# Kernel tuning notes

Measured on AMD Instinct MI355X. Metric: run time of the kernel, lower is better.

## Reference

```python
import jax, jax.numpy as jnp
import numpy as np


def _gcn_conv(x, src, dst, norm, W, b, n_nodes):
    # x: [N, Fin] -> [N, Fout]. PyG GCNConv: linear (no bias), normalized
    # scatter-add aggregation over edges (self-loops already in src/dst), + bias.
    h = x @ W                                  # [N, Fout]
    msg = h[src] * norm[:, None]               # [E+N, Fout]
    out = jax.ops.segment_sum(msg, dst, num_segments=n_nodes)
    return out + b


def _prep_edges(edge_index, n_nodes):
    # Add self-loops and compute symmetric normalization deg^-1/2 * deg^-1/2.
    loops = jnp.arange(n_nodes, dtype=edge_index.dtype)
    src = jnp.concatenate([edge_index[0], loops])
    dst = jnp.concatenate([edge_index[1], loops])
    deg = jax.ops.segment_sum(jnp.ones_like(dst, dtype=jnp.float32), dst,
                              num_segments=n_nodes)
    dinv = jnp.where(deg > 0, jax.lax.rsqrt(jnp.maximum(deg, 1.0)), 0.0)
    norm = dinv[src] * dinv[dst]
    return src, dst, norm


def setup_inputs() -> dict:
    key = jax.random.key(0)
    k1, k2, k3, k4 = jax.random.split(key, 4)
    N, Fin, Fout = 50000, 128, 64
    H = 2 * Fout
    E = 640000
    x = jax.random.normal(k1, (N, Fin), dtype=jnp.float32)
    edge_index = jax.random.randint(k2, (2, E), 0, N, dtype=jnp.int64)
    W1 = jax.random.normal(k3, (Fin, H), dtype=jnp.float32) * (1.0 / np.sqrt(Fin))
    b1 = jnp.zeros((H,), dtype=jnp.float32)
    W2 = jax.random.normal(k4, (H, Fout), dtype=jnp.float32) * (1.0 / np.sqrt(H))
    b2 = jnp.zeros((Fout,), dtype=jnp.float32)
    return {"x": x, "edge_index": edge_index, "W1": W1, "b1": b1, "W2": W2, "b2": b2}


def reference(x, edge_index, W1, b1, W2, b2):
    n_nodes = x.shape[0]
    src, dst, norm = _prep_edges(edge_index, n_nodes)
    h = _gcn_conv(x, src, dst, norm, W1, b1, n_nodes)
    h = jax.nn.relu(h)
    return _gcn_conv(h, src, dst, norm, W2, b2, n_nodes)
```

## Files before the change

### kernel.cpp

```cpp
#include <hip/hip_runtime.h>

#define CEILDIV(a,b) (((a)+(b)-1)/(b))

constexpr int BKCAP  = 1536;
constexpr int MAXBK  = 1024;
constexpr int CHUNKA = 4096;


__device__ __forceinline__ unsigned short f2bf(float f) {
  union { float f; unsigned u; } v; v.f = f;
  unsigned u = v.u + (0x7fffu + ((v.u >> 16) & 1u));
  return (unsigned short)(u >> 16);
}
__device__ __forceinline__ unsigned pack2(float lo, float hi) {
  return (unsigned)f2bf(lo) | ((unsigned)f2bf(hi) << 16);
}
__device__ __forceinline__ void add2(float* a, unsigned w) {
  union { unsigned u; float f; } lo, hi;
  lo.u = w << 16; hi.u = w & 0xffff0000u;
  a[0] += lo.f; a[1] += hi.f;
}
__device__ __forceinline__ void add8(float* a, uint4 w) {
  add2(a + 0, w.x); add2(a + 2, w.y); add2(a + 4, w.z); add2(a + 6, w.w);
}
__device__ __forceinline__ void fma2(float* a, unsigned w, float s) {
  union { unsigned u; float f; } lo, hi;
  lo.u = w << 16; hi.u = w & 0xffff0000u;
  a[0] = fmaf(lo.f, s, a[0]); a[1] = fmaf(hi.f, s, a[1]);
}
__device__ __forceinline__ void fma8(float* a, uint4 w, float s) {
  fma2(a + 0, w.x, s); fma2(a + 2, w.y, s); fma2(a + 4, w.z, s); fma2(a + 6, w.w, s);
}


__global__ __launch_bounds__(256) void k_init(const int* __restrict__ raw,
                                              int* __restrict__ ctrl, int E) {
  const int tid = threadIdx.x;
  for (int i = 1 + tid; i < 8 + MAXBK; i += 256) ctrl[i] = 0;
  __shared__ int ok;
  if (tid == 0) ok = 1;
  __syncthreads();
  int n = (E < 1024) ? E : 1024;
  for (int i = tid; i < n; i += 256)
    if (raw[2 * i + 1] != 0) ok = 0;
  __syncthreads();
  if (tid == 0) ctrl[0] = ok;
}

template <int K, int NO, bool XBF16, bool SCALE>
__device__ __forceinline__ void gemm_body(const void* __restrict__ Xv,
                                          const float* __restrict__ W,
                                          const int* __restrict__ cnt,
                                          unsigned short* __restrict__ Y,
                                          int N, int bid) {
  constexpr int ROWS = 128, KC = 16, TC = NO / 16;
  constexpr int XST = ROWS + 4;
  constexpr int WST = NO + 4;
  __shared__ float xs[KC * XST];
  __shared__ float ws[KC * WST];
  const int tid = threadIdx.x;
  const int tx = tid & 15, ty = tid >> 4;
  const int r0 = ty * 8;
  const int row0 = bid * ROWS;

  float acc[8][TC];
#pragma unroll
  for (int i = 0; i < 8; ++i)
#pragma unroll
    for (int j = 0; j < TC; ++j) acc[i][j] = 0.0f;

  for (int kk = 0; kk < K; kk += KC) {
#pragma unroll
    for (int it = 0; it < (ROWS * KC / 4) / 256; ++it) {
      int idx = it * 256 + tid;
      int r = idx >> 2, kq = idx & 3;
      int row = row0 + r; if (row >= N) row = N - 1;
      float f0, f1, f2, f3;
      if constexpr (XBF16) {
        const unsigned short* Xb = (const unsigned short*)Xv;
        uint2 v = *(const uint2*)&Xb[(size_t)row * K + kk + kq * 4];
        union { unsigned u; float f; } t0, t1, t2, t3;
        t0.u = v.x << 16; t1.u = v.x & 0xffff0000u;
        t2.u = v.y << 16; t3.u = v.y & 0xffff0000u;
        f0 = t0.f; f1 = t1.f; f2 = t2.f; f3 = t3.f;
      } else {
        const float* Xf = (const float*)Xv;
        float4 v = *(const float4*)&Xf[(size_t)row * K + kk + kq * 4];
        f0 = v.x; f1 = v.y; f2 = v.z; f3 = v.w;
      }
      xs[(kq * 4 + 0) * XST + r] = f0;
      xs[(kq * 4 + 1) * XST + r] = f1;
      xs[(kq * 4 + 2) * XST + r] = f2;
      xs[(kq * 4 + 3) * XST + r] = f3;
    }
#pragma unroll
    for (int it = 0; it < (KC * NO / 4) / 256; ++it) {
      int idx = it * 256 + tid;
      int c4 = idx & (NO / 4 - 1), kw = idx / (NO / 4);
      float4 v = *(const float4*)&W[(size_t)(kk + kw) * NO + c4 * 4];
      *(float4*)&ws[kw * WST + c4 * 4] = v;
    }
    __syncthreads();
#pragma unroll
    for (int k = 0; k < KC; ++k) {
      const float4 xa = *(const float4*)&xs[k * XST + r0];
      const float4 xb = *(const float4*)&xs[k * XST + r0 + 4];
      float4 wv[TC / 4];
      wv[0] = *(const float4*)&ws[k * WST + tx * 4];
      if constexpr (TC == 8)
        wv[1] = *(const float4*)&ws[k * WST + 64 + tx * 4];
      const float xr[8] = {xa.x, xa.y, xa.z, xa.w, xb.x, xb.y, xb.z, xb.w};
#pragma unroll
      for (int i = 0; i < 8; ++i)
#pragma unroll
        for (int j4 = 0; j4 < TC / 4; ++j4) {
          acc[i][j4 * 4 + 0] += xr[i] * wv[j4].x;
          acc[i][j4 * 4 + 1] += xr[i] * wv[j4].y;
          acc[i][j4 * 4 + 2] += xr[i] * wv[j4].z;
          acc[i][j4 * 4 + 3] += xr[i] * wv[j4].w;
        }
    }
    __syncthreads();
  }
#pragma unroll
  for (int i = 0; i < 8; ++i) {
    int r = row0 + r0 + i;
    if (r < N) {
      const float dv = SCALE ? rsqrtf((float)(cnt[r] + 1)) : 1.0f;
      uint2 pa = make_uint2(pack2(acc[i][0] * dv, acc[i][1] * dv),
                            pack2(acc[i][2] * dv, acc[i][3] * dv));
      *(uint2*)&Y[(size_t)r * NO + tx * 4] = pa;
      if constexpr (TC == 8) {
        uint2 pb = make_uint2(pack2(acc[i][4] * dv, acc[i][5] * dv),
                              pack2(acc[i][6] * dv, acc[i][7] * dv));
        *(uint2*)&Y[(size_t)r * NO + 64 + tx * 4] = pb;
      }
    }
  }
}

__global__ __launch_bounds__(256, 4) void k_work1(
    const float* __restrict__ X, const float* __restrict__ W1,
    unsigned short* __restrict__ hb1, int N, int FA,
    const int* __restrict__ raw, int* __restrict__ ctrl,
    unsigned* __restrict__ ebuf, int E, int nbk) {
  const int i = blockIdx.x;
  if (i >= FA) {
    gemm_body<128, 128, false, false>(X, W1, nullptr, hb1, N, i - FA);
    return;
  }
  __shared__ int lcnt[MAXBK], lbase[MAXBK], lrank[MAXBK];
  const int tid = threadIdx.x;
  for (int b = tid; b < nbk; b += 256) { lcnt[b] = 0; lrank[b] = 0; }
  __syncthreads();
  const bool is64 = (ctrl[0] != 0);
  const int e0 = i * CHUNKA;
  const int e1 = min(E, e0 + CHUNKA);
  for (int e = e0 + tid; e < e1; e += 256) {
    int d = is64 ? raw[2 * (E + e)] : raw[E + e];
    atomicAdd(&lcnt[d >> 6], 1);
  }
  __syncthreads();
  for (int b = tid; b < nbk; b += 256)
    if (lcnt[b]) lbase[b] = atomicAdd(&ctrl[8 + b], lcnt[b]);
  __syncthreads();
  for (int e = e0 + tid; e < e1; e += 256) {
    int s = is64 ? raw[2 * e] : raw[e];
    int d = is64 ? raw[2 * (E + e)] : raw[E + e];
    int bk = d >> 6;
    int r = atomicAdd(&lrank[bk], 1);
    int pos = lbase[bk] + r;
    if (pos < BKCAP)
      ebuf[(size_t)bk * BKCAP + pos] = (unsigned)s | ((unsigned)(d & 63) << 17);
  }
}

__global__ __launch_bounds__(256, 4) void k_work2(
    const float* __restrict__ X, const float* __restrict__ W1,
    unsigned short* __restrict__ hb1, int N, int NBK, int G1,
    const unsigned* __restrict__ ebuf, const int* __restrict__ ctrl,
    int* __restrict__ cnt, int* __restrict__ rowptr,
    int* __restrict__ esrc) {
  const int i = blockIdx.x;
  if (i >= NBK) {
    gemm_body<128, 128, false, false>(X, W1, nullptr, hb1, N, G1 + (i - NBK));
    return;
  }
  __shared__ int lcnt[64], lbase[64], lrank[64];
  const int tid = threadIdx.x;
  if (tid < 64) { lcnt[tid] = 0; lrank[tid] = 0; }
  __syncthreads();
  const int nb = min(ctrl[8 + i], BKCAP);
  const unsigned* __restrict__ eb = &ebuf[(size_t)i * BKCAP];
  for (int j = tid; j < nb; j += 256) atomicAdd(&lcnt[eb[j] >> 17], 1);
  __syncthreads();
  if (tid == 0) {
    int run = 0;
#pragma unroll
    for (int j = 0; j < 64; ++j) { lbase[j] = run; run += lcnt[j]; }
  }
  __syncthreads();
  if (tid < 64) {
    int v = i * 64 + tid;
    if (v < N) {
      cnt[v] = lcnt[tid];
      rowptr[v] = i * BKCAP + lbase[tid];
    }
  }
  for (int j = tid; j < nb; j += 256) {
    unsigned u = eb[j];
    int ld = (int)(u >> 17);
    int r = atomicAdd(&lrank[ld], 1);
    esrc[(size_t)i * BKCAP + lbase[ld] + r] = (int)(u & 0x1FFFFu);
  }
}

__global__ __launch_bounds__(256) void k_agg1(const unsigned short* __restrict__ h,
                                              const int* __restrict__ cnt,
                                              const int* __restrict__ rowptr,
                                              const int* __restrict__ esrc,
                                              const float* __restrict__ bias,
                                              unsigned short* __restrict__ out,
                                              int N) {
  const int v = blockIdx.x * 16 + (threadIdx.x >> 4);
  if (v >= N) return;
  const int lc = threadIdx.x & 15;
  const uint4* __restrict__ h4 = (const uint4*)h;

  const int deg = cnt[v];
  const float dv = rsqrtf((float)(deg + 1));
  float acc[8] = {0, 0, 0, 0, 0, 0, 0, 0};
  fma8(acc, h4[(size_t)v * 16 + lc], dv);
  const int* __restrict__ ep = &esrc[rowptr[v]];
  int e = 0;
  for (; e + 4 <= deg; e += 4) {
    int s0 = ep[e + 0], s1 = ep[e + 1], s2 = ep[e + 2], s3 = ep[e + 3];
    float w0 = rsqrtf((float)(cnt[s0] + 1));
    float w1 = rsqrtf((float)(cnt[s1] + 1));
    float w2 = rsqrtf((float)(cnt[s2] + 1));
    float w3 = rsqrtf((float)(cnt[s3] + 1));
    uint4 a0 = h4[(size_t)s0 * 16 + lc];
    uint4 a1 = h4[(size_t)s1 * 16 + lc];
    uint4 a2 = h4[(size_t)s2 * 16 + lc];
    uint4 a3 = h4[(size_t)s3 * 16 + lc];
    fma8(acc, a0, w0); fma8(acc, a1, w1); fma8(acc, a2, w2); fma8(acc, a3, w3);
  }
  for (; e < deg; ++e) {
    int s = ep[e];
    fma8(acc, h4[(size_t)s * 16 + lc], rsqrtf((float)(cnt[s] + 1)));
  }

  const float4 b0 = *(const float4*)&bias[lc * 8];
  const float4 b1 = *(const float4*)&bias[lc * 8 + 4];
  float r[8];
  r[0] = fmaxf(acc[0] * dv + b0.x, 0.0f);
  r[1] = fmaxf(acc[1] * dv + b0.y, 0.0f);
  r[2] = fmaxf(acc[2] * dv + b0.z, 0.0f);
  r[3] = fmaxf(acc[3] * dv + b0.w, 0.0f);
  r[4] = fmaxf(acc[4] * dv + b1.x, 0.0f);
  r[5] = fmaxf(acc[5] * dv + b1.y, 0.0f);
  r[6] = fmaxf(acc[6] * dv + b1.z, 0.0f);
  r[7] = fmaxf(acc[7] * dv + b1.w, 0.0f);
  uint4 pk = make_uint4(pack2(r[0], r[1]), pack2(r[2], r[3]),
                        pack2(r[4], r[5]), pack2(r[6], r[7]));
  ((uint4*)out)[(size_t)v * 16 + lc] = pk;
}

__global__ __launch_bounds__(256, 4) void k_gemm2(const unsigned short* __restrict__ X,
                                                  const float* __restrict__ W,
                                                  const int* __restrict__ cnt,
                                                  unsigned short* __restrict__ Y,
                                                  int N) {
  gemm_body<128, 64, true, true>(X, W, cnt, Y, N, blockIdx.x);
}

__global__ __launch_bounds__(256) void k_agg2(const unsigned short* __restrict__ h,
                                              const int* __restrict__ cnt,
                                              const int* __restrict__ rowptr,
                                              const int* __restrict__ esrc,
                                              const float* __restrict__ bias,
                                              float* __restrict__ out, int N) {
  constexpr int F = 64, LPN = 8, NPB = 32;
  const int v = blockIdx.x * NPB + threadIdx.x / LPN;
  if (v >= N) return;
  const int lc = threadIdx.x % LPN;
  const uint4* __restrict__ h4 = (const uint4*)h;

  float acc[8] = {0, 0, 0, 0, 0, 0, 0, 0};
  add8(acc, h4[(size_t)v * LPN + lc]);
  const int deg = cnt[v];
  const float dv = rsqrtf((float)(deg + 1));
  const int* __restrict__ ep = &esrc[rowptr[v]];
  int e = 0;
  for (; e + 4 <= deg; e += 4) {
    int s0 = ep[e + 0], s1 = ep[e + 1], s2 = ep[e + 2], s3 = ep[e + 3];
    uint4 a0 = h4[(size_t)s0 * LPN + lc];
    uint4 a1 = h4[(size_t)s1 * LPN + lc];
    uint4 a2 = h4[(size_t)s2 * LPN + lc];
    uint4 a3 = h4[(size_t)s3 * LPN + lc];
    add8(acc, a0); add8(acc, a1); add8(acc, a2); add8(acc, a3);
  }
  for (; e < deg; ++e) add8(acc, h4[(size_t)ep[e] * LPN + lc]);

  const float4 b0 = *(const float4*)&bias[lc * 8];
  const float4 b1 = *(const float4*)&bias[lc * 8 + 4];
  float4 o0, o1;
  o0.x = acc[0] * dv + b0.x; o0.y = acc[1] * dv + b0.y;
  o0.z = acc[2] * dv + b0.z; o0.w = acc[3] * dv + b0.w;
  o1.x = acc[4] * dv + b1.x; o1.y = acc[5] * dv + b1.y;
  o1.z = acc[6] * dv + b1.z; o1.w = acc[7] * dv + b1.w;
  float4* op = (float4*)(out + (size_t)v * F + lc * 8);
  op[0] = o0; op[1] = o1;
}


extern "C" void kernel_launch(void* const* d_in, const int* in_sizes, int n_in,
                              void* d_out, int out_size, void* d_ws, size_t ws_size,
                              hipStream_t stream) {
  const float* x  = (const float*)d_in[0];
  const int*   ei = (const int*)d_in[1];
  const float* W1 = (const float*)d_in[2];
  const float* b1 = (const float*)d_in[3];
  const float* W2 = (const float*)d_in[4];
  const float* b2 = (const float*)d_in[5];
  const int H    = in_sizes[3];
  const int Fin  = in_sizes[2] / H;
  const int N    = in_sizes[0] / Fin;
  const int E    = in_sizes[1] / 2;
  const int FO   = in_sizes[5];
  float* outp = (float*)d_out;

  const int NBK = CEILDIV(N, 64);
  const int FA  = CEILDIV(E, CHUNKA);
  const int GB  = CEILDIV(N, 128);
  const int G1  = (GB * 2) / 5;

  char* p = (char*)d_ws;
  auto alloc = [&](size_t bytes) {
    void* q = (void*)p;
    p += (bytes + 255) & ~(size_t)255;
    return q;
  };
  int*      ctrl   = (int*)alloc((8 + MAXBK) * 4);
  int*      cnt    = (int*)alloc((size_t)N * 4);
  int*      rowptr = (int*)alloc((size_t)N * 4);
  unsigned* ebuf   = (unsigned*)alloc((size_t)NBK * BKCAP * 4);
  int*      esrc   = (int*)alloc((size_t)NBK * BKCAP * 4);
  unsigned short* hb1 = (unsigned short*)alloc((size_t)N * H * 2);
  unsigned short* ab1 = (unsigned short*)alloc((size_t)N * H * 2);
  unsigned short* hb2 = (unsigned short*)alloc((size_t)N * FO * 2);

  k_init<<<1, 256, 0, stream>>>(ei, ctrl, E);
  k_work1<<<FA + G1, 256, 0, stream>>>(x, W1, hb1, N, FA, ei, ctrl, ebuf, E, NBK);
  k_work2<<<NBK + (GB - G1), 256, 0, stream>>>(x, W1, hb1, N, NBK, G1, ebuf,
                                               ctrl, cnt, rowptr, esrc);
  k_agg1<<<CEILDIV(N, 16), 256, 0, stream>>>(hb1, cnt, rowptr, esrc, b1, ab1, N);
  k_gemm2<<<CEILDIV(N, 128), 256, 0, stream>>>(ab1, W2, cnt, hb2, N);
  k_agg2<<<CEILDIV(N, 32), 256, 0, stream>>>(hb2, cnt, rowptr, esrc, b2, outp, N);
}
```

Before: 116.1 us.

## Share smem between gemm and bucketing, widen K chunk, vectorize edge reads

The GEMM K-chunk grows from 16 to 32 with a partial unroll, so there are half as many sync/load rounds per tile. The GEMM and bucketing paths now share one raw shared-memory buffer per kernel, so they no longer declare separate arrays. Edge index reads in the bucketing pass are vectorized four at a time when E is divisible by 4. The GEMM1 split between the two work kernels also moves from 2/5 to 1/2. Together these aim to cut load and sync overhead and rebalance overlap, at the cost of more shared memory per GEMM block and possibly lower occupancy.

```diff
diff --git a/kernel.cpp b/kernel.cpp
--- a/kernel.cpp
+++ b/kernel.cpp
@@ -48,16 +48,17 @@
 }
 
 template <int K, int NO, bool XBF16, bool SCALE>
-__device__ __forceinline__ void gemm_body(const void* __restrict__ Xv,
+__device__ __forceinline__ void gemm_body(char* smem_raw,
+                                          const void* __restrict__ Xv,
                                           const float* __restrict__ W,
                                           const int* __restrict__ cnt,
                                           unsigned short* __restrict__ Y,
                                           int N, int bid) {
-  constexpr int ROWS = 128, KC = 16, TC = NO / 16;
+  constexpr int ROWS = 128, KC = 32, TC = NO / 16;
   constexpr int XST = ROWS + 4;
   constexpr int WST = NO + 4;
-  __shared__ float xs[KC * XST];
-  __shared__ float ws[KC * WST];
+  float* xs = (float*)smem_raw;
+  float* ws = xs + KC * XST;
   const int tid = threadIdx.x;
   const int tx = tid & 15, ty = tid >> 4;
   const int r0 = ty * 8;
@@ -73,7 +74,7 @@
 #pragma unroll
     for (int it = 0; it < (ROWS * KC / 4) / 256; ++it) {
       int idx = it * 256 + tid;
-      int r = idx >> 2, kq = idx & 3;
+      int r = idx / (KC / 4), kq = idx % (KC / 4);
       int row = row0 + r; if (row >= N) row = N - 1;
       float f0, f1, f2, f3;
       if constexpr (XBF16) {
@@ -101,7 +102,7 @@
       *(float4*)&ws[kw * WST + c4 * 4] = v;
     }
     __syncthreads();
-#pragma unroll
+#pragma unroll 8
     for (int k = 0; k < KC; ++k) {
       const float4 xa = *(const float4*)&xs[k * XST + r0];
       const float4 xb = *(const float4*)&xs[k * XST + r0 + 4];
@@ -139,39 +140,90 @@
   }
 }
 
+constexpr int GEMM1_SMEM = (32 * 132 + 32 * 132) * 4;
+constexpr int GEMM2_SMEM = (32 * 132 + 32 * 68) * 4;
+
 __global__ __launch_bounds__(256, 4) void k_work1(
     const float* __restrict__ X, const float* __restrict__ W1,
     unsigned short* __restrict__ hb1, int N, int FA,
     const int* __restrict__ raw, int* __restrict__ ctrl,
     unsigned* __restrict__ ebuf, int E, int nbk) {
+  __shared__ __align__(16) char smem[GEMM1_SMEM];
   const int i = blockIdx.x;
   if (i >= FA) {
-    gemm_body<128, 128, false, false>(X, W1, nullptr, hb1, N, i - FA);
+    gemm_body<128, 128, false, false>(smem, X, W1, nullptr, hb1, N, i - FA);
     return;
   }
-  __shared__ int lcnt[MAXBK], lbase[MAXBK], lrank[MAXBK];
+  int* lcnt  = (int*)smem;
+  int* lbase = lcnt + MAXBK;
+  int* lrank = lbase + MAXBK;
   const int tid = threadIdx.x;
   for (int b = tid; b < nbk; b += 256) { lcnt[b] = 0; lrank[b] = 0; }
   __syncthreads();
   const bool is64 = (ctrl[0] != 0);
   const int e0 = i * CHUNKA;
   const int e1 = min(E, e0 + CHUNKA);
-  for (int e = e0 + tid; e < e1; e += 256) {
-    int d = is64 ? raw[2 * (E + e)] : raw[E + e];
-    atomicAdd(&lcnt[d >> 6], 1);
-  }
-  __syncthreads();
-  for (int b = tid; b < nbk; b += 256)
-    if (lcnt[b]) lbase[b] = atomicAdd(&ctrl[8 + b], lcnt[b]);
-  __syncthreads();
-  for (int e = e0 + tid; e < e1; e += 256) {
-    int s = is64 ? raw[2 * e] : raw[e];
-    int d = is64 ? raw[2 * (E + e)] : raw[E + e];
-    int bk = d >> 6;
-    int r = atomicAdd(&lrank[bk], 1);
-    int pos = lbase[bk] + r;
-    if (pos < BKCAP)
-      ebuf[(size_t)bk * BKCAP + pos] = (unsigned)s | ((unsigned)(d & 63) << 17);
+  if ((E & 3) == 0) {
+    for (int e = e0 + tid * 4; e < e1; e += 1024) {
+      int d0, d1, d2, d3;
+      if (is64) {
+        uint4 a = *(const uint4*)&raw[2 * (E + e)];
+        uint4 b = *(const uint4*)&raw[2 * (E + e) + 4];
+        d0 = (int)a.x; d1 = (int)a.z; d2 = (int)b.x; d3 = (int)b.z;
+      } else {
+        uint4 v = *(const uint4*)&raw[E + e];
+        d0 = (int)v.x; d1 = (int)v.y; d2 = (int)v.z; d3 = (int)v.w;
+      }
+      atomicAdd(&lcnt[d0 >> 6], 1); atomicAdd(&lcnt[d1 >> 6], 1);
+      atomicAdd(&lcnt[d2 >> 6], 1); atomicAdd(&lcnt[d3 >> 6], 1);
+    }
+    __syncthreads();
+    for (int b = tid; b < nbk; b += 256)
+      if (lcnt[b]) lbase[b] = atomicAdd(&ctrl[8 + b], lcnt[b]);
+    __syncthreads();
+    for (int e = e0 + tid * 4; e < e1; e += 1024) {
+      int s[4], d[4];
+      if (is64) {
+        uint4 sa = *(const uint4*)&raw[2 * e];
+        uint4 sb = *(const uint4*)&raw[2 * e + 4];
+        uint4 da = *(const uint4*)&raw[2 * (E + e)];
+        uint4 db = *(const uint4*)&raw[2 * (E + e) + 4];
+        s[0] = (int)sa.x; s[1] = (int)sa.z; s[2] = (int)sb.x; s[3] = (int)sb.z;
+        d[0] = (int)da.x; d[1] = (int)da.z; d[2] = (int)db.x; d[3] = (int)db.z;
+      } else {
+        uint4 sv = *(const uint4*)&raw[e];
+        uint4 dv = *(const uint4*)&raw[E + e];
+        s[0] = (int)sv.x; s[1] = (int)sv.y; s[2] = (int)sv.z; s[3] = (int)sv.w;
+        d[0] = (int)dv.x; d[1] = (int)dv.y; d[2] = (int)dv.z; d[3] = (int)dv.w;
+      }
+#pragma unroll
+      for (int j = 0; j < 4; ++j) {
+        int bk = d[j] >> 6;
+        int r = atomicAdd(&lrank[bk], 1);
+        int pos = lbase[bk] + r;
+        if (pos < BKCAP)
+          ebuf[(size_t)bk * BKCAP + pos] =
+              (unsigned)s[j] | ((unsigned)(d[j] & 63) << 17);
+      }
+    }
+  } else {
+    for (int e = e0 + tid; e < e1; e += 256) {
+      int d = is64 ? raw[2 * (E + e)] : raw[E + e];
+      atomicAdd(&lcnt[d >> 6], 1);
+    }
+    __syncthreads();
+    for (int b = tid; b < nbk; b += 256)
+      if (lcnt[b]) lbase[b] = atomicAdd(&ctrl[8 + b], lcnt[b]);
+    __syncthreads();
+    for (int e = e0 + tid; e < e1; e += 256) {
+      int s = is64 ? raw[2 * e] : raw[e];
+      int d = is64 ? raw[2 * (E + e)] : raw[E + e];
+      int bk = d >> 6;
+      int r = atomicAdd(&lrank[bk], 1);
+      int pos = lbase[bk] + r;
+      if (pos < BKCAP)
+        ebuf[(size_t)bk * BKCAP + pos] = (unsigned)s | ((unsigned)(d & 63) << 17);
+    }
   }
 }
 
@@ -181,12 +233,16 @@
     const unsigned* __restrict__ ebuf, const int* __restrict__ ctrl,
     int* __restrict__ cnt, int* __restrict__ rowptr,
     int* __restrict__ esrc) {
+  __shared__ __align__(16) char smem[GEMM1_SMEM];
   const int i = blockIdx.x;
   if (i >= NBK) {
-    gemm_body<128, 128, false, false>(X, W1, nullptr, hb1, N, G1 + (i - NBK));
+    gemm_body<128, 128, false, false>(smem, X, W1, nullptr, hb1, N,
+                                      G1 + (i - NBK));
     return;
   }
-  __shared__ int lcnt[64], lbase[64], lrank[64];
+  int* lcnt  = (int*)smem;
+  int* lbase = lcnt + 64;
+  int* lrank = lbase + 64;
   const int tid = threadIdx.x;
   if (tid < 64) { lcnt[tid] = 0; lrank[tid] = 0; }
   __syncthreads();
@@ -271,7 +327,8 @@
                                                   const int* __restrict__ cnt,
                                                   unsigned short* __restrict__ Y,
                                                   int N) {
-  gemm_body<128, 64, true, true>(X, W, cnt, Y, N, blockIdx.x);
+  __shared__ __align__(16) char smem[GEMM2_SMEM];
+  gemm_body<128, 64, true, true>(smem, X, W, cnt, Y, N, blockIdx.x);
 }
 
 __global__ __launch_bounds__(256) void k_agg2(const unsigned short* __restrict__ h,
@@ -333,7 +390,7 @@
   const int NBK = CEILDIV(N, 64);
   const int FA  = CEILDIV(E, CHUNKA);
   const int GB  = CEILDIV(N, 128);
-  const int G1  = (GB * 2) / 5;
+  const int G1  = GB / 2;
 
   char* p = (char*)d_ws;
   auto alloc = [&](size_t bytes) {
```

Result: slower. 129.8 us (+11.7%).
